# Performance work log

Measured on AMD Instinct MI355X. Metric: run time of the kernel, lower is better.

Reference implementation:

```python
import jax, jax.numpy as jnp
import numpy as np

B, T, S, F, H, V = 4, 160, 80, 640, 1024, 1024

def setup_inputs() -> dict:
    key = jax.random.key(0)
    ks = jax.random.split(key, 4)
    return {
        "source_encodings": jax.random.normal(ks[0], (B, T, F), dtype=jnp.float32),
        "target_encodings": jax.random.normal(ks[1], (B, S, F), dtype=jnp.float32),
        "W1": jax.random.normal(ks[2], (F, H), dtype=jnp.float32) * (1.0 / np.sqrt(F)),
        "b1": jnp.zeros((H,), dtype=jnp.float32),
        "W2": jax.random.normal(ks[3], (H, V), dtype=jnp.float32) * (1.0 / np.sqrt(H)),
        "b2": jnp.zeros((V,), dtype=jnp.float32),
    }

def reference(source_encodings, target_encodings, W1, b1, W2, b2):
    # broadcast add: [B,T,1,F] + [B,1,S,F] -> [B,T,S,F]
    combined = source_encodings[:, :, None, :] + target_encodings[:, None, :, :]
    # FFN: Linear -> ReLU -> Linear (dropout=0 / eval)
    h = jax.nn.relu(jnp.einsum("btsf,fh->btsh", combined, W1) + b1)
    logits = jnp.einsum("btsh,hv->btsv", h, W2) + b2
    # eval mode applies log_softmax over vocab
    return jax.nn.log_softmax(logits, axis=-1)
```

## Files before the change

kernel.cpp:

```cpp
#include <hip/hip_runtime.h>
#include <type_traits>
#include <utility>

#define B_ 4
#define T_ 160
#define S_ 80
#define F_ 640
#define H_ 1024
#define V_ 1024

typedef float f32x4 __attribute__((ext_vector_type(4)));
typedef short s16x8 __attribute__((ext_vector_type(8)));
typedef __bf16 bf16x8_t __attribute__((ext_vector_type(8)));

template <typename T, typename = void>
struct MfmaTakes : std::false_type {};
template <typename T>
struct MfmaTakes<T, std::void_t<decltype(__builtin_amdgcn_mfma_f32_16x16x32_bf16(
    std::declval<T>(), std::declval<T>(), std::declval<f32x4>(), 0, 0, 0))>>
    : std::true_type {};

template <typename S8>
__device__ __forceinline__ f32x4 mfma_bf16_16x16x32(S8 a, S8 b, f32x4 c) {
  if constexpr (MfmaTakes<S8>::value) {
    return __builtin_amdgcn_mfma_f32_16x16x32_bf16(a, b, c, 0, 0, 0);
  } else {
    return __builtin_amdgcn_mfma_f32_16x16x32_bf16(
        __builtin_bit_cast(bf16x8_t, a), __builtin_bit_cast(bf16x8_t, b), c, 0, 0, 0);
  }
}

__device__ __forceinline__ unsigned short f2bf(float x) {
  unsigned int u = __float_as_uint(x);
  u += 0x7FFFu + ((u >> 16) & 1u);
  return (unsigned short)(u >> 16);
}

__global__ __launch_bounds__(256) void prep_weights(const float* __restrict__ W1,
                                                    const float* __restrict__ W2,
                                                    s16x8* __restrict__ W1p,
                                                    s16x8* __restrict__ W2p) {
  const int NW1 = (F_ / 8) * H_;
  const int NW2 = (H_ / 8) * V_;
  int c = blockIdx.x * 256 + threadIdx.x;
  if (c < NW1) {
    int kg = c >> 10, v = c & 1023;
    s16x8 o;
#pragma unroll
    for (int i = 0; i < 8; ++i) o[i] = (short)f2bf(W1[(kg * 8 + i) * H_ + v]);
    W1p[c] = o;
  } else if (c < NW1 + NW2) {
    int c2 = c - NW1;
    int kg = c2 >> 10, v = c2 & 1023;
    s16x8 o;
#pragma unroll
    for (int i = 0; i < 8; ++i) o[i] = (short)f2bf(W2[(kg * 8 + i) * V_ + v]);
    W2p[c2] = o;
  }
}

__global__ __launch_bounds__(512, 2) void pq_gemm(const float* __restrict__ src,
                                                  const float* __restrict__ tgt,
                                                  const s16x8* __restrict__ W1p,
                                                  const float* __restrict__ b1,
                                                  float* __restrict__ P,
                                                  float* __restrict__ Q) {
  __shared__ s16x8 a_lds[64 * 80];
  const int tid = threadIdx.x;
  const int wr = blockIdx.x;
  const int r0 = wr * 64;
  const bool isP = (wr < 10);

  for (int c = tid; c < 64 * 80; c += 512) {
    int m = c / 80, kg8 = c - m * 80;
    int R = r0 + m;
    const float* rowp = isP ? (src + R * F_) : (tgt + (R - 640) * F_);
    const f32x4* p4 = (const f32x4*)(rowp + kg8 * 8);
    f32x4 x0 = p4[0], x1 = p4[1];
    s16x8 o;
#pragma unroll
    for (int i = 0; i < 4; ++i) o[i] = (short)f2bf(x0[i]);
#pragma unroll
    for (int i = 0; i < 4; ++i) o[4 + i] = (short)f2bf(x1[i]);
    a_lds[m * 80 + (kg8 ^ (m & 7))] = o;
  }
  __syncthreads();

  const int l = tid & 63, wv = tid >> 6;
  const int g = l >> 4, cl = l & 15;
  const f32x4 zero = {0.f, 0.f, 0.f, 0.f};
  f32x4 acc[4][8];
#pragma unroll
  for (int rt = 0; rt < 4; ++rt)
#pragma unroll
    for (int ct = 0; ct < 8; ++ct) acc[rt][ct] = zero;

  const s16x8* bbase = W1p + g * 1024 + wv * 128 + cl;
  s16x8 bA[8], bB[8], af[4];
#pragma unroll
  for (int ct = 0; ct < 8; ++ct) bA[ct] = bbase[ct * 16];

  for (int ks = 0; ks < 20; ks += 2) {
#pragma unroll
    for (int ct = 0; ct < 8; ++ct) bB[ct] = bbase[(ks + 1) * 4096 + ct * 16];
#pragma unroll
    for (int rt = 0; rt < 4; ++rt) {
      int m = rt * 16 + cl;
      af[rt] = a_lds[m * 80 + ((ks * 4 + g) ^ (m & 7))];
    }
#pragma unroll
    for (int ct = 0; ct < 8; ++ct)
#pragma unroll
      for (int rt = 0; rt < 4; ++rt)
        acc[rt][ct] = mfma_bf16_16x16x32(af[rt], bA[ct], acc[rt][ct]);
    int ksn = (ks + 2 < 20) ? (ks + 2) : 0;
#pragma unroll
    for (int ct = 0; ct < 8; ++ct) bA[ct] = bbase[ksn * 4096 + ct * 16];
#pragma unroll
    for (int rt = 0; rt < 4; ++rt) {
      int m = rt * 16 + cl;
      af[rt] = a_lds[m * 80 + (((ks + 1) * 4 + g) ^ (m & 7))];
    }
#pragma unroll
    for (int ct = 0; ct < 8; ++ct)
#pragma unroll
      for (int rt = 0; rt < 4; ++rt)
        acc[rt][ct] = mfma_bf16_16x16x32(af[rt], bB[ct], acc[rt][ct]);
  }

  float b1v[8];
#pragma unroll
  for (int ct = 0; ct < 8; ++ct) b1v[ct] = isP ? b1[wv * 128 + ct * 16 + cl] : 0.f;
  float* outbase = isP ? P : Q;
  const int orow0 = isP ? r0 : (r0 - 640);
#pragma unroll
  for (int rt = 0; rt < 4; ++rt) {
#pragma unroll
    for (int j = 0; j < 4; ++j) {
      int row = rt * 16 + g * 4 + j;
      float* op = outbase + (size_t)(orow0 + row) * H_ + wv * 128 + cl;
#pragma unroll
      for (int ct = 0; ct < 8; ++ct) op[ct * 16] = acc[rt][ct][j] + b1v[ct];
    }
  }
}

__global__ __launch_bounds__(1024, 4) void joint_main(const float* __restrict__ Pm,
                                                      const float* __restrict__ Qm,
                                                      const s16x8* __restrict__ W2p,
                                                      const float* __restrict__ b2,
                                                      float* __restrict__ out) {
  __shared__ s16x8 h_lds[64 * 129];
  const int tid = threadIdx.x;
  int bx = blockIdx.x;
  int bid = (bx & 7) * 100 + (bx >> 3);
  const int b = bid / 200;
  int rem = bid - b * 200;
  const int t0 = (rem / 10) * 8;
  const int s0 = (rem - (rem / 10) * 10) * 8;

  for (int c = tid; c < 64 * 128; c += 1024) {
    int m = c >> 7, kg8 = c & 127;
    int dt = m >> 3, ds = m & 7;
    const f32x4* p4 = (const f32x4*)(Pm + (size_t)(b * T_ + t0 + dt) * H_ + kg8 * 8);
    const f32x4* q4 = (const f32x4*)(Qm + (size_t)(b * S_ + s0 + ds) * H_ + kg8 * 8);
    f32x4 x0 = p4[0] + q4[0];
    f32x4 x1 = p4[1] + q4[1];
    s16x8 o;
#pragma unroll
    for (int i = 0; i < 4; ++i) o[i] = (short)f2bf(fmaxf(x0[i], 0.f));
#pragma unroll
    for (int i = 0; i < 4; ++i) o[4 + i] = (short)f2bf(fmaxf(x1[i], 0.f));
    h_lds[m * 129 + kg8] = o;
  }
  __syncthreads();

  const int l = tid & 63, wv = tid >> 6;
  const int g = l >> 4, cl = l & 15;
  f32x4 acc[4][4];
#pragma unroll
  for (int rt = 0; rt < 4; ++rt)
#pragma unroll
    for (int ct = 0; ct < 4; ++ct) acc[rt][ct] = {0.f, 0.f, 0.f, 0.f};

  const s16x8* bb = W2p + g * 1024 + wv * 64 + cl;
  const s16x8* a0p = h_lds + (0 * 16 + cl) * 129 + g;
  const s16x8* a1p = h_lds + (1 * 16 + cl) * 129 + g;
  const s16x8* a2p = h_lds + (2 * 16 + cl) * 129 + g;
  const s16x8* a3p = h_lds + (3 * 16 + cl) * 129 + g;

#pragma unroll 4
  for (int ks = 0; ks < 32; ++ks) {
    const s16x8* base = bb + ks * 4096;
    s16x8 bf0 = base[0];
    s16x8 bf1 = base[16];
    s16x8 bf2 = base[32];
    s16x8 bf3 = base[48];
    s16x8 a0 = a0p[ks * 4];
    s16x8 a1 = a1p[ks * 4];
    s16x8 a2 = a2p[ks * 4];
    s16x8 a3 = a3p[ks * 4];
    acc[0][0] = mfma_bf16_16x16x32(a0, bf0, acc[0][0]);
    acc[1][0] = mfma_bf16_16x16x32(a1, bf0, acc[1][0]);
    acc[2][0] = mfma_bf16_16x16x32(a2, bf0, acc[2][0]);
    acc[3][0] = mfma_bf16_16x16x32(a3, bf0, acc[3][0]);
    acc[0][1] = mfma_bf16_16x16x32(a0, bf1, acc[0][1]);
    acc[1][1] = mfma_bf16_16x16x32(a1, bf1, acc[1][1]);
    acc[2][1] = mfma_bf16_16x16x32(a2, bf1, acc[2][1]);
    acc[3][1] = mfma_bf16_16x16x32(a3, bf1, acc[3][1]);
    acc[0][2] = mfma_bf16_16x16x32(a0, bf2, acc[0][2]);
    acc[1][2] = mfma_bf16_16x16x32(a1, bf2, acc[1][2]);
    acc[2][2] = mfma_bf16_16x16x32(a2, bf2, acc[2][2]);
    acc[3][2] = mfma_bf16_16x16x32(a3, bf2, acc[3][2]);
    acc[0][3] = mfma_bf16_16x16x32(a0, bf3, acc[0][3]);
    acc[1][3] = mfma_bf16_16x16x32(a1, bf3, acc[1][3]);
    acc[2][3] = mfma_bf16_16x16x32(a2, bf3, acc[2][3]);
    acc[3][3] = mfma_bf16_16x16x32(a3, bf3, acc[3][3]);
  }

  __syncthreads();
  float* redm = reinterpret_cast<float*>(h_lds);
  float* reds = redm + 1024;
  float* gmbuf = reds + 1024;
  float* lsebuf = gmbuf + 64;

#pragma unroll
  for (int ct = 0; ct < 4; ++ct) {
    float bv = b2[wv * 64 + ct * 16 + cl];
#pragma unroll
    for (int rt = 0; rt < 4; ++rt)
#pragma unroll
      for (int j = 0; j < 4; ++j) acc[rt][ct][j] += bv;
  }

#pragma unroll
  for (int rt = 0; rt < 4; ++rt)
#pragma unroll
    for (int j = 0; j < 4; ++j) {
      float mx = fmaxf(fmaxf(acc[rt][0][j], acc[rt][1][j]),
                       fmaxf(acc[rt][2][j], acc[rt][3][j]));
#pragma unroll
      for (int msk = 1; msk < 16; msk <<= 1) mx = fmaxf(mx, __shfl_xor(mx, msk, 64));
      if (cl == 0) redm[wv * 64 + rt * 16 + g * 4 + j] = mx;
    }
  __syncthreads();

  if (tid < 64) {
    float mx = redm[tid];
#pragma unroll
    for (int w = 1; w < 16; ++w) mx = fmaxf(mx, redm[w * 64 + tid]);
    gmbuf[tid] = mx;
  }
  __syncthreads();

#pragma unroll
  for (int rt = 0; rt < 4; ++rt)
#pragma unroll
    for (int j = 0; j < 4; ++j) {
      int row = rt * 16 + g * 4 + j;
      float gm = gmbuf[row];
      float ps = __expf(acc[rt][0][j] - gm) + __expf(acc[rt][1][j] - gm) +
                 __expf(acc[rt][2][j] - gm) + __expf(acc[rt][3][j] - gm);
#pragma unroll
      for (int msk = 1; msk < 16; msk <<= 1) ps += __shfl_xor(ps, msk, 64);
      if (cl == 0) reds[wv * 64 + row] = ps;
    }
  __syncthreads();

  if (tid < 64) {
    float s = reds[tid];
#pragma unroll
    for (int w = 1; w < 16; ++w) s += reds[w * 64 + tid];
    lsebuf[tid] = gmbuf[tid] + __logf(s);
  }
  __syncthreads();

#pragma unroll
  for (int rt = 0; rt < 4; ++rt)
#pragma unroll
    for (int j = 0; j < 4; ++j) {
      int row = rt * 16 + g * 4 + j;
      float lse = lsebuf[row];
      int n = (b * T_ + t0 + (row >> 3)) * S_ + s0 + (row & 7);
      float* op = out + (size_t)n * V_ + wv * 64 + cl;
#pragma unroll
      for (int ct = 0; ct < 4; ++ct) op[ct * 16] = acc[rt][ct][j] - lse;
    }
}

extern "C" void kernel_launch(void* const* d_in, const int* in_sizes, int n_in,
                              void* d_out, int out_size, void* d_ws, size_t ws_size,
                              hipStream_t stream) {
  const float* src = (const float*)d_in[0];
  const float* tgt = (const float*)d_in[1];
  const float* W1  = (const float*)d_in[2];
  const float* b1  = (const float*)d_in[3];
  const float* W2  = (const float*)d_in[4];
  const float* b2  = (const float*)d_in[5];
  float* out = (float*)d_out;

  char* ws = (char*)d_ws;
  s16x8* W1p = (s16x8*)(ws);
  s16x8* W2p = (s16x8*)(ws + 1310720);
  float* P   = (float*)(ws + 3407872);
  float* Q   = (float*)(ws + 6029312);

  prep_weights<<<832, 256, 0, stream>>>(W1, W2, W1p, W2p);
  pq_gemm<<<15, 512, 0, stream>>>(src, tgt, W1p, b1, P, Q);
  joint_main<<<800, 1024, 0, stream>>>(P, Q, W2p, b2, out);
}
```

Baseline: 209.3 us.

## Split joint kernel into tiled logits GEMM plus separate log-softmax pass

Replaces the fused 64-row x full-vocab kernel with a logits GEMM using 256x128 output tiles. The hidden activations are built per k-slice into double-buffered LDS, so each W2 column tile is reused across 256 rows instead of 64. Log-softmax moves to a second kernel that re-reads and rewrites the full 52 MB logits tensor. This trades fused normalization for extra global memory traffic, and also adds a barrier per k-step and rebuilds the activations once per column tile.

```diff
diff --git a/kernel.cpp b/kernel.cpp
--- a/kernel.cpp
+++ b/kernel.cpp
@@ -145,61 +145,71 @@
   }
 }
 
-__global__ __launch_bounds__(1024, 4) void joint_main(const float* __restrict__ Pm,
+__global__ __launch_bounds__(512, 2) void logits_gemm(const float* __restrict__ Pm,
                                                       const float* __restrict__ Qm,
                                                       const s16x8* __restrict__ W2p,
                                                       const float* __restrict__ b2,
                                                       float* __restrict__ out) {
-  __shared__ s16x8 h_lds[64 * 129];
+  __shared__ s16x8 h_lds[2][256 * 5];
   const int tid = threadIdx.x;
   int bx = blockIdx.x;
-  int bid = (bx & 7) * 100 + (bx >> 3);
-  const int b = bid / 200;
-  int rem = bid - b * 200;
-  const int t0 = (rem / 10) * 8;
-  const int s0 = (rem - (rem / 10) * 10) * 8;
-
-  for (int c = tid; c < 64 * 128; c += 1024) {
-    int m = c >> 7, kg8 = c & 127;
-    int dt = m >> 3, ds = m & 7;
-    const f32x4* p4 = (const f32x4*)(Pm + (size_t)(b * T_ + t0 + dt) * H_ + kg8 * 8);
-    const f32x4* q4 = (const f32x4*)(Qm + (size_t)(b * S_ + s0 + ds) * H_ + kg8 * 8);
-    f32x4 x0 = p4[0] + q4[0];
-    f32x4 x1 = p4[1] + q4[1];
-    s16x8 o;
-#pragma unroll
-    for (int i = 0; i < 4; ++i) o[i] = (short)f2bf(fmaxf(x0[i], 0.f));
-#pragma unroll
-    for (int i = 0; i < 4; ++i) o[4 + i] = (short)f2bf(fmaxf(x1[i], 0.f));
-    h_lds[m * 129 + kg8] = o;
-  }
-  __syncthreads();
+  int wg = (bx & 7) * 200 + (bx >> 3);
+  const int rowtile = wg >> 3, coltile = wg & 7;
+  const int b = rowtile / 50;
+  int rr = rowtile - b * 50;
+  const int t0 = (rr / 10) * 32;
+  const int s0 = (rr - (rr / 10) * 10) * 8;
 
   const int l = tid & 63, wv = tid >> 6;
   const int g = l >> 4, cl = l & 15;
+  const int wr = wv >> 1, wc = wv & 1;
+
   f32x4 acc[4][4];
 #pragma unroll
   for (int rt = 0; rt < 4; ++rt)
 #pragma unroll
     for (int ct = 0; ct < 4; ++ct) acc[rt][ct] = {0.f, 0.f, 0.f, 0.f};
 
-  const s16x8* bb = W2p + g * 1024 + wv * 64 + cl;
-  const s16x8* a0p = h_lds + (0 * 16 + cl) * 129 + g;
-  const s16x8* a1p = h_lds + (1 * 16 + cl) * 129 + g;
-  const s16x8* a2p = h_lds + (2 * 16 + cl) * 129 + g;
-  const s16x8* a3p = h_lds + (3 * 16 + cl) * 129 + g;
-
-#pragma unroll 4
+  const s16x8* bb = W2p + g * 1024 + coltile * 128 + wc * 64 + cl;
+  const int arow = (wr * 64 + cl) * 5 + g;
+
+#define BUILD(ks, bsel)                                                         \
+  {                                                                             \
+    _Pragma("unroll")                                                           \
+    for (int i = 0; i < 2; ++i) {                                               \
+      int c = tid + 512 * i;                                                    \
+      int row = c >> 2, kg = c & 3;                                             \
+      int dt = row >> 3, ds = row & 7;                                          \
+      const f32x4* p4 = (const f32x4*)(Pm + (size_t)(b * T_ + t0 + dt) * H_ +   \
+                                       (ks) * 32 + kg * 8);                     \
+      const f32x4* q4 = (const f32x4*)(Qm + (size_t)(b * S_ + s0 + ds) * H_ +   \
+                                       (ks) * 32 + kg * 8);                     \
+      f32x4 x0 = p4[0] + q4[0];                                                 \
+      f32x4 x1 = p4[1] + q4[1];                                                 \
+      s16x8 o;                                                                  \
+      _Pragma("unroll")                                                         \
+      for (int e = 0; e < 4; ++e) o[e] = (short)f2bf(fmaxf(x0[e], 0.f));        \
+      _Pragma("unroll")                                                         \
+      for (int e = 0; e < 4; ++e) o[4 + e] = (short)f2bf(fmaxf(x1[e], 0.f));    \
+      h_lds[bsel][row * 5 + kg] = o;                                            \
+    }                                                                           \
+  }
+
+  BUILD(0, 0);
+  __syncthreads();
+
   for (int ks = 0; ks < 32; ++ks) {
+    if (ks + 1 < 32) BUILD(ks + 1, (ks + 1) & 1);
     const s16x8* base = bb + ks * 4096;
     s16x8 bf0 = base[0];
     s16x8 bf1 = base[16];
     s16x8 bf2 = base[32];
     s16x8 bf3 = base[48];
-    s16x8 a0 = a0p[ks * 4];
-    s16x8 a1 = a1p[ks * 4];
-    s16x8 a2 = a2p[ks * 4];
-    s16x8 a3 = a3p[ks * 4];
+    const s16x8* ap = &h_lds[ks & 1][arow];
+    s16x8 a0 = ap[0];
+    s16x8 a1 = ap[16 * 5];
+    s16x8 a2 = ap[32 * 5];
+    s16x8 a3 = ap[48 * 5];
     acc[0][0] = mfma_bf16_16x16x32(a0, bf0, acc[0][0]);
     acc[1][0] = mfma_bf16_16x16x32(a1, bf0, acc[1][0]);
     acc[2][0] = mfma_bf16_16x16x32(a2, bf0, acc[2][0]);
@@ -216,76 +226,58 @@
     acc[1][3] = mfma_bf16_16x16x32(a1, bf3, acc[1][3]);
     acc[2][3] = mfma_bf16_16x16x32(a2, bf3, acc[2][3]);
     acc[3][3] = mfma_bf16_16x16x32(a3, bf3, acc[3][3]);
-  }
-
-  __syncthreads();
-  float* redm = reinterpret_cast<float*>(h_lds);
-  float* reds = redm + 1024;
-  float* gmbuf = reds + 1024;
-  float* lsebuf = gmbuf + 64;
-
-#pragma unroll
-  for (int ct = 0; ct < 4; ++ct) {
-    float bv = b2[wv * 64 + ct * 16 + cl];
-#pragma unroll
-    for (int rt = 0; rt < 4; ++rt)
-#pragma unroll
-      for (int j = 0; j < 4; ++j) acc[rt][ct][j] += bv;
-  }
-
+    __syncthreads();
+  }
+#undef BUILD
+
+  float bv[4];
+#pragma unroll
+  for (int ct = 0; ct < 4; ++ct) bv[ct] = b2[coltile * 128 + wc * 64 + ct * 16 + cl];
 #pragma unroll
   for (int rt = 0; rt < 4; ++rt)
 #pragma unroll
     for (int j = 0; j < 4; ++j) {
-      float mx = fmaxf(fmaxf(acc[rt][0][j], acc[rt][1][j]),
-                       fmaxf(acc[rt][2][j], acc[rt][3][j]));
-#pragma unroll
-      for (int msk = 1; msk < 16; msk <<= 1) mx = fmaxf(mx, __shfl_xor(mx, msk, 64));
-      if (cl == 0) redm[wv * 64 + rt * 16 + g * 4 + j] = mx;
+      int row256 = wr * 64 + rt * 16 + g * 4 + j;
+      int dt = row256 >> 3, ds = row256 & 7;
+      int n = (b * T_ + t0 + dt) * S_ + s0 + ds;
+      float* op = out + (size_t)n * V_ + coltile * 128 + wc * 64 + cl;
+#pragma unroll
+      for (int ct = 0; ct < 4; ++ct) op[ct * 16] = acc[rt][ct][j] + bv[ct];
     }
-  __syncthreads();
-
-  if (tid < 64) {
-    float mx = redm[tid];
-#pragma unroll
-    for (int w = 1; w < 16; ++w) mx = fmaxf(mx, redm[w * 64 + tid]);
-    gmbuf[tid] = mx;
-  }
-  __syncthreads();
-
-#pragma unroll
-  for (int rt = 0; rt < 4; ++rt)
-#pragma unroll
-    for (int j = 0; j < 4; ++j) {
-      int row = rt * 16 + g * 4 + j;
-      float gm = gmbuf[row];
-      float ps = __expf(acc[rt][0][j] - gm) + __expf(acc[rt][1][j] - gm) +
-                 __expf(acc[rt][2][j] - gm) + __expf(acc[rt][3][j] - gm);
-#pragma unroll
-      for (int msk = 1; msk < 16; msk <<= 1) ps += __shfl_xor(ps, msk, 64);
-      if (cl == 0) reds[wv * 64 + row] = ps;
-    }
-  __syncthreads();
-
-  if (tid < 64) {
-    float s = reds[tid];
-#pragma unroll
-    for (int w = 1; w < 16; ++w) s += reds[w * 64 + tid];
-    lsebuf[tid] = gmbuf[tid] + __logf(s);
-  }
-  __syncthreads();
-
-#pragma unroll
-  for (int rt = 0; rt < 4; ++rt)
-#pragma unroll
-    for (int j = 0; j < 4; ++j) {
-      int row = rt * 16 + g * 4 + j;
-      float lse = lsebuf[row];
-      int n = (b * T_ + t0 + (row >> 3)) * S_ + s0 + (row & 7);
-      float* op = out + (size_t)n * V_ + wv * 64 + cl;
-#pragma unroll
-      for (int ct = 0; ct < 4; ++ct) op[ct * 16] = acc[rt][ct][j] - lse;
-    }
+}
+
+__global__ __launch_bounds__(256) void lse_sub(float* __restrict__ out) {
+  const int wv = threadIdx.x >> 6, l = threadIdx.x & 63;
+  const size_t n = (size_t)blockIdx.x * 4 + wv;
+  float* row = out + n * V_;
+  f32x4 v[4];
+#pragma unroll
+  for (int i = 0; i < 4; ++i) v[i] = ((const f32x4*)row)[l + 64 * i];
+
+  float m = v[0][0];
+#pragma unroll
+  for (int i = 0; i < 4; ++i)
+#pragma unroll
+    for (int j = 0; j < 4; ++j) m = fmaxf(m, v[i][j]);
+#pragma unroll
+  for (int msk = 1; msk < 64; msk <<= 1) m = fmaxf(m, __shfl_xor(m, msk, 64));
+
+  float s = 0.f;
+#pragma unroll
+  for (int i = 0; i < 4; ++i)
+#pragma unroll
+    for (int j = 0; j < 4; ++j) s += __expf(v[i][j] - m);
+#pragma unroll
+  for (int msk = 1; msk < 64; msk <<= 1) s += __shfl_xor(s, msk, 64);
+
+  const float lse = m + __logf(s);
+#pragma unroll
+  for (int i = 0; i < 4; ++i) {
+    f32x4 o = v[i];
+#pragma unroll
+    for (int j = 0; j < 4; ++j) o[j] -= lse;
+    ((f32x4*)row)[l + 64 * i] = o;
+  }
 }
 
 extern "C" void kernel_launch(void* const* d_in, const int* in_sizes, int n_in,
@@ -307,5 +299,6 @@
 
   prep_weights<<<832, 256, 0, stream>>>(W1, W2, W1p, W2p);
   pq_gemm<<<15, 512, 0, stream>>>(src, tgt, W1p, b1, P, Q);
-  joint_main<<<800, 1024, 0, stream>>>(P, Q, W2p, b2, out);
-}
+  logits_gemm<<<1600, 512, 0, stream>>>(P, Q, W2p, b2, out);
+  lse_sub<<<12800, 256, 0, stream>>>(out);
+}
```

Measured after the change: 278.9 us. 1.33x slower.
